# Optimization experiments

Hardware: AMD Instinct MI355X
Metric: run time of the kernel (lower is better)

Reference implementation:

```python
import jax, jax.numpy as jnp
import numpy as np

M = 5            # Anderson memory
LAM = 1e-4       # Tikhonov regularization on Gram matrix
MAX_ITER = 50
TOL = 0.01
BETA = 1.0
BSZ, DIM = 64, 4096


def f_layer(z, x, W, b):
    # canonical DEQ cell: contraction so the fixed point exists
    return jnp.tanh(z @ W + x + b)


def anderson(f, x0, m=M, lam=LAM, max_iter=MAX_ITER, tol=TOL, beta=BETA):
    """Anderson acceleration; faithful port of DEQFixedPoint.anderson.
    Variable history length n=min(k,m) is handled by masking so the whole
    loop is jit-compatible (lax.while_loop with early stop on tol)."""
    bsz = x0.shape[0]
    d = int(np.prod(x0.shape[1:]))
    ff = lambda v: f(v.reshape(x0.shape)).reshape(bsz, d)
    x0f = x0.reshape(bsz, d)

    X = jnp.zeros((bsz, m, d), x0.dtype)
    F = jnp.zeros((bsz, m, d), x0.dtype)
    F0 = ff(x0f)
    F1 = ff(F0)
    X = X.at[:, 0].set(x0f).at[:, 1].set(F0)
    F = F.at[:, 0].set(F0).at[:, 1].set(F1)

    y = jnp.zeros((bsz, m + 1, 1), x0.dtype).at[:, 0, 0].set(1.0)
    eye_m = jnp.eye(m, dtype=x0.dtype)

    def cond(state):
        _, _, k, res = state
        return (k < max_iter) & (res >= tol)

    def body(state):
        X, F, k, res = state
        n = jnp.minimum(k, m)
        mask = (jnp.arange(m) < n).astype(x0.dtype)          # active history slots
        G = (F - X) * mask[None, :, None]                     # (bsz, m, d)
        GG = jnp.einsum('bmd,bnd->bmn', G, G)                 # small 5x5 Gram
        # masked (n+1)x(n+1) subproblem embedded in (m+1)x(m+1): inactive
        # rows become identity rows with zero rhs -> alpha_i = 0 for i >= n,
        # exactly matching torch's solve on the leading (n+1) block.
        Hin = (GG + lam * eye_m) * (mask[:, None] * mask[None, :]) + jnp.diag(1.0 - mask)
        H = jnp.zeros((bsz, m + 1, m + 1), x0.dtype)
        H = H.at[:, 0, 1:].set(mask).at[:, 1:, 0].set(mask).at[:, 1:, 1:].set(Hin)
        alpha = jnp.linalg.solve(H, y)[:, 1:, 0]              # (bsz, m)
        Xk = beta * jnp.einsum('bm,bmd->bd', alpha, F) + (1.0 - beta) * jnp.einsum('bm,bmd->bd', alpha, X)
        Fk = ff(Xk)
        idx = k % m
        Xn = X.at[:, idx].set(Xk)
        Fn = F.at[:, idx].set(Fk)
        r = jnp.linalg.norm(Fk - Xk) / (1e-5 + jnp.linalg.norm(Fk))
        return Xn, Fn, k + 1, r

    init = (X, F, jnp.array(2, jnp.int32), jnp.array(jnp.inf, x0.dtype))
    X, F, k, res = jax.lax.while_loop(cond, body, init)
    idx = (k - 1) % m  # k was incremented after the last executed iteration
    return X[:, idx].reshape(x0.shape)


def setup_inputs():
    key = jax.random.key(0)
    kx, kw, kb = jax.random.split(key, 3)
    x = jax.random.normal(kx, (BSZ, DIM), jnp.float32)
    # spectral norm of W ~ 2 * 0.4 = 0.8 -> contraction through tanh
    W = jax.random.normal(kw, (DIM, DIM), jnp.float32) * (0.4 / np.sqrt(DIM))
    b = jax.random.normal(kb, (DIM,), jnp.float32) * 0.1
    return {"x": x, "W": W, "b": b}


def reference(x, W, b):
    # forward: solve z* = f(z*, x) with no grad, then one grad-carrying f step
    zstar = anderson(lambda z: f_layer(z, x, W, b), jnp.zeros_like(x))
    return f_layer(zstar, x, W, b)
```

## Files before the change

kernel.cpp:

```cpp
#include <hip/hip_runtime.h>

#define NBLK 256
#define GBLK 128
#define NTHR 1024
#define BSZ 64
#define DIM 4096
#define MEM 5
#define MAXIT 50
#define TOL_ 0.01f
#define LAM_ 1e-4f

#define X_OFF 0
#define F_OFF (BSZ * MEM * DIM)
#define Z_OFF (2 * BSZ * MEM * DIM)
#define RP_OFF (Z_OFF + BSZ * DIM)
#define BAR_OFF (RP_OFF + 640)
#define FP32_WS_FLOATS (RP_OFF + 1024)
#define ZF_BYTE ((size_t)(RP_OFF + 1024) * 4)
#define WF_BYTE (ZF_BYTE + (size_t)BSZ * DIM * 2)
#define WS_NEED (WF_BYTE + (size_t)DIM * DIM * 2)

typedef __attribute__((ext_vector_type(8))) _Float16 half8v;
typedef __attribute__((ext_vector_type(4))) float f32x4;

__device__ __forceinline__ unsigned short f2h(float f) {
    _Float16 h = (_Float16)f;
    unsigned short u;
    __builtin_memcpy(&u, &h, 2);
    return u;
}

__device__ __forceinline__ void gridbar(unsigned int* flags, unsigned int* go,
                                        unsigned int e)
{
    __syncthreads();
    const int tid = threadIdx.x;
    if (blockIdx.x == 0) {
        if (tid == 0) {
            __builtin_amdgcn_fence(__ATOMIC_RELEASE, "agent");
            __hip_atomic_store(&flags[0], e, __ATOMIC_RELAXED,
                               __HIP_MEMORY_SCOPE_AGENT);
        }
        if (tid < NBLK) {
            while (__hip_atomic_load(&flags[tid], __ATOMIC_RELAXED,
                                     __HIP_MEMORY_SCOPE_AGENT) < e)
                __builtin_amdgcn_s_sleep(1);
        }
        __syncthreads();
        if (tid == 0) {
            __builtin_amdgcn_fence(__ATOMIC_ACQUIRE, "agent");
            __hip_atomic_store(go, e, __ATOMIC_RELAXED,
                               __HIP_MEMORY_SCOPE_AGENT);
        }
    } else {
        if (tid == 0) {
            __builtin_amdgcn_fence(__ATOMIC_RELEASE, "agent");
            __hip_atomic_store(&flags[blockIdx.x], e, __ATOMIC_RELAXED,
                               __HIP_MEMORY_SCOPE_AGENT);
            while (__hip_atomic_load(go, __ATOMIC_RELAXED,
                                     __HIP_MEMORY_SCOPE_AGENT) < e)
                __builtin_amdgcn_s_sleep(1);
            __builtin_amdgcn_fence(__ATOMIC_ACQUIRE, "agent");
        }
    }
    __syncthreads();
}

__device__ void convert_w(const float* __restrict__ W, unsigned short* __restrict__ Wf,
                          float* smem)
{
    const int tid = threadIdx.x;
    const int blk = blockIdx.x;
    const int jc = blk << 4;
    for (int sc = 0; sc < 8; ++sc) {
        __syncthreads();
        #pragma unroll
        for (int h = 0; h < 2; ++h) {
            int rrow = (tid >> 2) + (h << 8);
            int seg = tid & 3;
            float4 v = *(const float4*)&W[(size_t)((sc << 9) + rrow) * DIM + jc + (seg << 2)];
            float* dst = smem + rrow * 17 + (seg << 2);
            dst[0] = v.x; dst[1] = v.y; dst[2] = v.z; dst[3] = v.w;
        }
        __syncthreads();
        unsigned int* of = (unsigned int*)(Wf + ((size_t)blk * 128 + sc * 16) * 512);
        #pragma unroll
        for (int it = 0; it < 4; ++it) {
            int o = tid + (it << 10);
            int ksl = o >> 8, ln = (o >> 2) & 63, ep = o & 3;
            int kl = (ksl << 5) + ((ln >> 4) << 3) + (ep << 1);
            float w0 = smem[kl * 17 + (ln & 15)];
            float w1 = smem[(kl + 1) * 17 + (ln & 15)];
            of[o] = (unsigned int)f2h(w0) | ((unsigned int)f2h(w1) << 16);
        }
    }
    __syncthreads();
}

__device__ __forceinline__ void gemm_tanh_mfma(
    int idx, const float* __restrict__ x, const float* __restrict__ bias,
    const unsigned short* __restrict__ Zf, const unsigned short* __restrict__ Wf,
    float* __restrict__ Z, float* __restrict__ Fs, float* __restrict__ rp, float* smem)
{
    const int tid = threadIdx.x;
    const int cb = blockIdx.x;
    const int lane = tid & 63;
    const int w = tid >> 6;
    const int r0 = lane & 15;
    const int kg = lane >> 4;
    f32x4 acc[4][2] = {};

    const unsigned short* b0 = Wf + (size_t)(cb * 2) * 65536;
    const unsigned short* b1 = Wf + (size_t)(cb * 2 + 1) * 65536;
    const int ksbase = w << 3;

    #pragma unroll 2
    for (int s = 0; s < 8; ++s) {
        const int ks = ksbase + s;
        const size_t bo = ((size_t)ks << 9) + (lane << 3);
        half8v B0 = *(const half8v*)(b0 + bo);
        half8v B1 = *(const half8v*)(b1 + bo);
        const int kbase = (ks << 5) + (kg << 3);
        #pragma unroll
        for (int m = 0; m < 4; ++m) {
            const size_t ao = (size_t)((m << 4) + r0) * DIM + kbase;
            half8v Ah = *(const half8v*)(Zf + ao);
            acc[m][0] = __builtin_amdgcn_mfma_f32_16x16x32_f16(Ah, B0, acc[m][0], 0, 0, 0);
            acc[m][1] = __builtin_amdgcn_mfma_f32_16x16x32_f16(Ah, B1, acc[m][1], 0, 0, 0);
        }
    }
    const int row = tid >> 4, cc = tid & 15;
    const int m_o = row >> 4, rl = row & 15;
    const int lsrc = cc + ((rl >> 2) << 4), reg = rl & 3;
    float sum0 = 0.f, sum1 = 0.f;
    #pragma unroll
    for (int rnd = 0; rnd < 4; ++rnd) {
        __syncthreads();
        if ((w >> 2) == rnd) {
            float* sec = smem + (w & 3) * 2052;
            #pragma unroll
            for (int m = 0; m < 4; ++m) {
                *(f32x4*)(sec + ((m * 2 + 0) << 8) + (lane << 2)) = acc[m][0];
                *(f32x4*)(sec + ((m * 2 + 1) << 8) + (lane << 2)) = acc[m][1];
            }
        }
        __syncthreads();
        #pragma unroll
        for (int p = 0; p < 4; ++p) {
            sum0 += smem[p * 2052 + ((m_o * 2 + 0) << 8) + (lsrc << 2) + reg];
            sum1 += smem[p * 2052 + ((m_o * 2 + 1) << 8) + (lsrc << 2) + reg];
        }
    }
    const int j0 = (cb << 5) + cc;
    const int j1 = j0 + 16;
    float fz0 = tanhf(sum0 + x[(row << 12) + j0] + bias[j0]);
    float fz1 = tanhf(sum1 + x[(row << 12) + j1] + bias[j1]);
    Fs[(row * MEM + idx) * DIM + j0] = fz0;
    Fs[(row * MEM + idx) * DIM + j1] = fz1;
    float d0 = fz0 - Z[(row << 12) + j0];
    float d1 = fz1 - Z[(row << 12) + j1];
    float lnum = d0 * d0 + d1 * d1;
    float lden = fz0 * fz0 + fz1 * fz1;
    #pragma unroll
    for (int off = 1; off < 64; off <<= 1) {
        lnum += __shfl_xor(lnum, off, 64);
        lden += __shfl_xor(lden, off, 64);
    }
    if (lane == 0) { smem[8448 + w] = lnum; smem[8480 + w] = lden; }
    __syncthreads();
    if (tid == 0) {
        float a = 0.f, b2 = 0.f;
        #pragma unroll
        for (int i = 0; i < 16; ++i) { a += smem[8448 + i]; b2 += smem[8480 + i]; }
        rp[cb] = a;
        rp[NBLK + cb] = b2;
    }
}

__device__ __forceinline__ void gemm_tanh_fp32(
    int idx, const float* __restrict__ x, const float* __restrict__ W,
    const float* __restrict__ bias, float* __restrict__ wsf, float* smem)
{
    const int tid = threadIdx.x;
    const int blk = blockIdx.x;
    const int lane = tid & 63;
    const int w = tid >> 6;
    const int r = w >> 2;
    const int q = w & 3;
    const int jcq = (blk << 4) + (q << 2);
    float* Z = wsf + Z_OFF;
    float* Fs = wsf + F_OFF;
    float* rp = wsf + RP_OFF;

    float acc0 = 0.f, acc1 = 0.f, acc2 = 0.f, acc3 = 0.f;
    const int lx = lane & 15;
    const float* inrow = smem + (r << 12) + (lane << 6);
    const int srow = tid >> 4;
    const int sg = tid & 15;

    for (int step = 0; step < 16; ++step) {
        #pragma unroll
        for (int i = 0; i < 4; ++i) {
            float4 v = *(const float4*)&Z[srow * DIM + (i << 10) + (step << 6) + (sg << 2)];
            *(float4*)&smem[(i << 12) + (srow << 6) + ((sg ^ (srow & 15)) << 2)] = v;
        }
        __syncthreads();
        const float* wbase = W + (size_t)((r << 10) + (step << 6)) * DIM + jcq;
        #pragma unroll 2
        for (int s = 0; s < 16; ++s) {
            float4 in4 = *(const float4*)&inrow[(s ^ lx) << 2];
            const float* wr = wbase + (size_t)(s << 2) * DIM;
            #pragma unroll
            for (int t = 0; t < 4; ++t) {
                float iv = (t == 0) ? in4.x : (t == 1) ? in4.y : (t == 2) ? in4.z : in4.w;
                float4 wq = *(const float4*)(wr + (size_t)t * DIM);
                acc0 = fmaf(iv, wq.x, acc0);
                acc1 = fmaf(iv, wq.y, acc1);
                acc2 = fmaf(iv, wq.z, acc2);
                acc3 = fmaf(iv, wq.w, acc3);
            }
        }
        __syncthreads();
    }
    {
        float* rrow = smem + r * 1088 + lane * 17 + (q << 2);
        rrow[0] = acc0; rrow[1] = acc1; rrow[2] = acc2; rrow[3] = acc3;
    }
    __syncthreads();
    const int row = tid >> 4, cc = tid & 15;
    const int boff = row * 17 + cc;
    float sum = smem[boff] + smem[1088 + boff] + smem[2176 + boff] + smem[3264 + boff];
    const int j = (blk << 4) + cc;
    float fz = tanhf(sum + x[(row << 12) + j] + bias[j]);
    Fs[(row * MEM + idx) * DIM + j] = fz;
    float d = fz - Z[(row << 12) + j];
    float lnum = d * d, lden = fz * fz;
    #pragma unroll
    for (int off = 1; off < 64; off <<= 1) {
        lnum += __shfl_xor(lnum, off, 64);
        lden += __shfl_xor(lden, off, 64);
    }
    if (lane == 0) { smem[8448 + w] = lnum; smem[8480 + w] = lden; }
    __syncthreads();
    if (tid == 0) {
        float a = 0.f, b2 = 0.f;
        for (int i = 0; i < 16; ++i) { a += smem[8448 + i]; b2 += smem[8480 + i]; }
        rp[blk] = a;
        rp[NBLK + blk] = b2;
    }
}

__device__ __forceinline__ float phase_res(const float* __restrict__ rp, float* smem)
{
    const int tid = threadIdx.x;
    const int lane = tid & 63, w = tid >> 6;
    float a = (tid < NBLK) ? rp[tid] : 0.f;
    float b = (tid < NBLK) ? rp[NBLK + tid] : 0.f;
    #pragma unroll
    for (int off = 1; off < 64; off <<= 1) {
        a += __shfl_xor(a, off, 64);
        b += __shfl_xor(b, off, 64);
    }
    if (lane == 0) { smem[w] = a; smem[16 + w] = b; }
    __syncthreads();
    if (tid == 0) {
        float sa = 0.f, sb = 0.f;
        for (int i = 0; i < 16; ++i) { sa += smem[i]; sb += smem[16 + i]; }
        smem[32] = sqrtf(sa) / (1e-5f + sqrtf(sb));
    }
    __syncthreads();
    float res = smem[32];
    __syncthreads();
    return res;
}

template <bool F16>
__device__ void gram_solve_combine(int b, int n, int idx, float* __restrict__ wsf,
                                   unsigned short* __restrict__ Zf, float* smem)
{
    const int tid = threadIdx.x;
    const int lane = tid & 63, w = tid >> 6;
    float* Xs = wsf + X_OFF;
    float* Fs = wsf + F_OFF;
    float* Z = wsf + Z_OFF;
    const int j4 = tid << 2;

    float g[MEM][4];
    #pragma unroll
    for (int i = 0; i < MEM; ++i) {
        float4 fv = *(const float4*)&Fs[(b * MEM + i) * DIM + j4];
        float4 xv = *(const float4*)&Xs[(b * MEM + i) * DIM + j4];
        bool act = (i < n);
        g[i][0] = act ? (fv.x - xv.x) : 0.f;
        g[i][1] = act ? (fv.y - xv.y) : 0.f;
        g[i][2] = act ? (fv.z - xv.z) : 0.f;
        g[i][3] = act ? (fv.w - xv.w) : 0.f;
    }
    float gg[15];
    {
        int p = 0;
        #pragma unroll
        for (int i = 0; i < MEM; ++i)
            #pragma unroll
            for (int qq = i; qq < MEM; ++qq) {
                float s = 0.f;
                #pragma unroll
                for (int c = 0; c < 4; ++c) s = fmaf(g[i][c], g[qq][c], s);
                gg[p++] = s;
            }
    }
    #pragma unroll
    for (int off = 1; off < 64; off <<= 1)
        #pragma unroll
        for (int p = 0; p < 15; ++p) gg[p] += __shfl_xor(gg[p], off, 64);
    if (lane == 0) {
        #pragma unroll
        for (int p = 0; p < 15; ++p) smem[p * 16 + w] = gg[p];
    }
    __syncthreads();
    if (tid == 0) {
        float G[MEM][MEM];
        int p = 0;
        for (int i = 0; i < MEM; ++i)
            for (int qq = i; qq < MEM; ++qq) {
                float v = 0.f;
                for (int ww = 0; ww < 16; ++ww) v += smem[p * 16 + ww];
                G[i][qq] = v; G[qq][i] = v; ++p;
            }
        float H[6][6], yv[6];
        for (int i = 0; i < 6; ++i) yv[i] = (i == 0) ? 1.f : 0.f;
        H[0][0] = 0.f;
        for (int i = 0; i < MEM; ++i) {
            float mi = (i < n) ? 1.f : 0.f;
            H[0][1 + i] = mi;
            H[1 + i][0] = mi;
        }
        for (int i = 0; i < MEM; ++i)
            for (int qq = 0; qq < MEM; ++qq) {
                float v;
                if (i < n && qq < n) v = G[i][qq] + ((i == qq) ? LAM_ : 0.f);
                else v = (i == qq) ? 1.f : 0.f;
                H[1 + i][1 + qq] = v;
            }
        for (int col = 0; col < 6; ++col) {
            int piv = col;
            float mv = fabsf(H[col][col]);
            for (int rr = col + 1; rr < 6; ++rr) {
                float av = fabsf(H[rr][col]);
                if (av > mv) { mv = av; piv = rr; }
            }
            if (piv != col) {
                for (int c2 = 0; c2 < 6; ++c2) { float tv = H[col][c2]; H[col][c2] = H[piv][c2]; H[piv][c2] = tv; }
                float tv = yv[col]; yv[col] = yv[piv]; yv[piv] = tv;
            }
            float pv = H[col][col];
            for (int rr = col + 1; rr < 6; ++rr) {
                float f = H[rr][col] / pv;
                H[rr][col] = 0.f;
                for (int c2 = col + 1; c2 < 6; ++c2) H[rr][c2] -= f * H[col][c2];
                yv[rr] -= f * yv[col];
            }
        }
        float sol[6];
        for (int col = 5; col >= 0; --col) {
            float s = yv[col];
            for (int c2 = col + 1; c2 < 6; ++c2) s -= H[col][c2] * sol[c2];
            sol[col] = s / H[col][col];
        }
        for (int i = 0; i < MEM; ++i) smem[240 + i] = sol[1 + i];
    }
    __syncthreads();
    float al[MEM];
    #pragma unroll
    for (int i = 0; i < MEM; ++i) al[i] = smem[240 + i];
    float4 zf = {0.f, 0.f, 0.f, 0.f};
    #pragma unroll
    for (int i = 0; i < MEM; ++i) {
        float4 fv = *(const float4*)&Fs[(b * MEM + i) * DIM + j4];
        zf.x = fmaf(al[i], fv.x, zf.x);
        zf.y = fmaf(al[i], fv.y, zf.y);
        zf.z = fmaf(al[i], fv.z, zf.z);
        zf.w = fmaf(al[i], fv.w, zf.w);
    }
    *(float4*)&Z[(b << 12) + j4] = zf;
    *(float4*)&Xs[(b * MEM + idx) * DIM + j4] = zf;
    if constexpr (F16) {
        unsigned int* z16 = (unsigned int*)(Zf + ((size_t)b << 12) + j4);
        z16[0] = (unsigned int)f2h(zf.x) | ((unsigned int)f2h(zf.y) << 16);
        z16[1] = (unsigned int)f2h(zf.z) | ((unsigned int)f2h(zf.w) << 16);
    }
}

template <bool F16>
__global__ __launch_bounds__(NTHR, 4)
void deq_anderson(const float* __restrict__ x, const float* __restrict__ W,
                  const float* __restrict__ bias, float* __restrict__ out,
                  char* __restrict__ ws)
{
    __shared__ __align__(16) float smem[16384];
    float* wsf = (float*)ws;
    unsigned int* flags = (unsigned int*)(wsf + BAR_OFF);
    unsigned int* go = flags + 272;
    unsigned short* Zf = (unsigned short*)(ws + ZF_BYTE);
    unsigned short* Wf = (unsigned short*)(ws + WF_BYTE);
    const int tid = threadIdx.x;
    const int blk = blockIdx.x;
    const int e = blk * NTHR + tid;
    const int b = e >> 12, j = e & (DIM - 1);
    float* Xs = wsf + X_OFF;
    float* Fs = wsf + F_OFF;
    float* Z = wsf + Z_OFF;
    float* rp = wsf + RP_OFF;
    unsigned int ep = 1;

    {
        float f0 = tanhf(x[e] + bias[j]);
        #pragma unroll
        for (int i = 0; i < MEM; ++i) {
            Xs[(b * MEM + i) * DIM + j] = (i == 1) ? f0 : 0.f;
            Fs[(b * MEM + i) * DIM + j] = (i == 0) ? f0 : 0.f;
        }
        Z[e] = f0;
        if constexpr (F16) Zf[e] = f2h(f0);
    }
    if constexpr (F16) convert_w(W, Wf, smem);
    gridbar(flags, go, ep++);
    if constexpr (F16) {
        if (blk < GBLK)
            gemm_tanh_mfma(1, x, bias, Zf, Wf, Z, Fs, rp, smem);
        else if (tid == 0) { rp[blk] = 0.f; rp[NBLK + blk] = 0.f; }
    } else {
        gemm_tanh_fp32(1, x, W, bias, wsf, smem);
    }
    gridbar(flags, go, ep++);

    int kend = MAXIT;
    for (int k = 2; k < MAXIT; ++k) {
        float res = phase_res(rp, smem);
        if (k > 2 && res < TOL_) { kend = k; break; }
        const int n = (k < MEM) ? k : MEM;
        const int idx = k % MEM;
        if (blk < BSZ) gram_solve_combine<F16>(blk, n, idx, wsf, Zf, smem);
        gridbar(flags, go, ep++);
        if constexpr (F16) {
            if (blk < GBLK)
                gemm_tanh_mfma(idx, x, bias, Zf, Wf, Z, Fs, rp, smem);
        } else {
            gemm_tanh_fp32(idx, x, W, bias, wsf, smem);
        }
        gridbar(flags, go, ep++);
    }

    const int fidx = (kend - 1) % MEM;
    out[e] = Fs[(b * MEM + fidx) * DIM + j];
}

extern "C" void kernel_launch(void* const* d_in, const int* in_sizes, int n_in,
                              void* d_out, int out_size, void* d_ws, size_t ws_size,
                              hipStream_t stream)
{
    (void)in_sizes; (void)n_in; (void)out_size;
    if (ws_size < (size_t)FP32_WS_FLOATS * sizeof(float)) return;
    const float* x = (const float*)d_in[0];
    const float* W = (const float*)d_in[1];
    const float* b = (const float*)d_in[2];
    float* out = (float*)d_out;
    char* ws = (char*)d_ws;
    hipMemsetAsync(ws + (size_t)BAR_OFF * 4, 0, 1152, stream);
    void* args[] = {(void*)&x, (void*)&W, (void*)&b, (void*)&out, (void*)&ws};
    const void* fn = (ws_size >= WS_NEED)
                         ? reinterpret_cast<const void*>(&deq_anderson<true>)
                         : reinterpret_cast<const void*>(&deq_anderson<false>);
    hipLaunchCooperativeKernel(fn, dim3(NBLK), dim3(NTHR), args, 0, stream);
}
```

Before: 240.4 us.

## Replace two-level grid barrier with all-to-all flag polling; keep F rows in registers

The grid barrier no longer routes through block 0 and a separate go flag. Every block now publishes its epoch flag and polls all 256 flags directly, which removes one serialized round trip per barrier. In exchange, all blocks now generate polling traffic on the shared flag array. Separately, the Anderson combine reuses the F history values already loaded for the Gram computation instead of reloading them from global memory, at the cost of extra registers.

```diff
diff --git a/kernel.cpp b/kernel.cpp
--- a/kernel.cpp
+++ b/kernel.cpp
@@ -30,39 +30,23 @@
     return u;
 }
 
-__device__ __forceinline__ void gridbar(unsigned int* flags, unsigned int* go,
-                                        unsigned int e)
-{
-    __syncthreads();
-    const int tid = threadIdx.x;
-    if (blockIdx.x == 0) {
-        if (tid == 0) {
-            __builtin_amdgcn_fence(__ATOMIC_RELEASE, "agent");
-            __hip_atomic_store(&flags[0], e, __ATOMIC_RELAXED,
-                               __HIP_MEMORY_SCOPE_AGENT);
-        }
-        if (tid < NBLK) {
-            while (__hip_atomic_load(&flags[tid], __ATOMIC_RELAXED,
-                                     __HIP_MEMORY_SCOPE_AGENT) < e)
-                __builtin_amdgcn_s_sleep(1);
-        }
-        __syncthreads();
-        if (tid == 0) {
-            __builtin_amdgcn_fence(__ATOMIC_ACQUIRE, "agent");
-            __hip_atomic_store(go, e, __ATOMIC_RELAXED,
-                               __HIP_MEMORY_SCOPE_AGENT);
-        }
-    } else {
-        if (tid == 0) {
-            __builtin_amdgcn_fence(__ATOMIC_RELEASE, "agent");
-            __hip_atomic_store(&flags[blockIdx.x], e, __ATOMIC_RELAXED,
-                               __HIP_MEMORY_SCOPE_AGENT);
-            while (__hip_atomic_load(go, __ATOMIC_RELAXED,
-                                     __HIP_MEMORY_SCOPE_AGENT) < e)
-                __builtin_amdgcn_s_sleep(1);
-            __builtin_amdgcn_fence(__ATOMIC_ACQUIRE, "agent");
-        }
-    }
+__device__ __forceinline__ void gridbar(unsigned int* flags, unsigned int e)
+{
+    __syncthreads();
+    const int tid = threadIdx.x;
+    if (tid == 0) {
+        __builtin_amdgcn_fence(__ATOMIC_RELEASE, "agent");
+        __hip_atomic_store(&flags[blockIdx.x], e, __ATOMIC_RELAXED,
+                           __HIP_MEMORY_SCOPE_AGENT);
+    }
+    if (tid < NBLK) {
+        while (__hip_atomic_load(&flags[tid], __ATOMIC_RELAXED,
+                                 __HIP_MEMORY_SCOPE_AGENT) < e)
+            __builtin_amdgcn_s_sleep(1);
+    }
+    __syncthreads();
+    if (tid == 0)
+        __builtin_amdgcn_fence(__ATOMIC_ACQUIRE, "agent");
     __syncthreads();
 }
 
@@ -285,16 +269,18 @@
     float* Z = wsf + Z_OFF;
     const int j4 = tid << 2;
 
+    float fv[MEM][4];
     float g[MEM][4];
     #pragma unroll
     for (int i = 0; i < MEM; ++i) {
-        float4 fv = *(const float4*)&Fs[(b * MEM + i) * DIM + j4];
+        float4 f4 = *(const float4*)&Fs[(b * MEM + i) * DIM + j4];
         float4 xv = *(const float4*)&Xs[(b * MEM + i) * DIM + j4];
+        fv[i][0] = f4.x; fv[i][1] = f4.y; fv[i][2] = f4.z; fv[i][3] = f4.w;
         bool act = (i < n);
-        g[i][0] = act ? (fv.x - xv.x) : 0.f;
-        g[i][1] = act ? (fv.y - xv.y) : 0.f;
-        g[i][2] = act ? (fv.z - xv.z) : 0.f;
-        g[i][3] = act ? (fv.w - xv.w) : 0.f;
+        g[i][0] = act ? (f4.x - xv.x) : 0.f;
+        g[i][1] = act ? (f4.y - xv.y) : 0.f;
+        g[i][2] = act ? (f4.z - xv.z) : 0.f;
+        g[i][3] = act ? (f4.w - xv.w) : 0.f;
     }
     float gg[15];
     {
@@ -376,11 +362,10 @@
     float4 zf = {0.f, 0.f, 0.f, 0.f};
     #pragma unroll
     for (int i = 0; i < MEM; ++i) {
-        float4 fv = *(const float4*)&Fs[(b * MEM + i) * DIM + j4];
-        zf.x = fmaf(al[i], fv.x, zf.x);
-        zf.y = fmaf(al[i], fv.y, zf.y);
-        zf.z = fmaf(al[i], fv.z, zf.z);
-        zf.w = fmaf(al[i], fv.w, zf.w);
+        zf.x = fmaf(al[i], fv[i][0], zf.x);
+        zf.y = fmaf(al[i], fv[i][1], zf.y);
+        zf.z = fmaf(al[i], fv[i][2], zf.z);
+        zf.w = fmaf(al[i], fv[i][3], zf.w);
     }
     *(float4*)&Z[(b << 12) + j4] = zf;
     *(float4*)&Xs[(b * MEM + idx) * DIM + j4] = zf;
@@ -400,7 +385,6 @@
     __shared__ __align__(16) float smem[16384];
     float* wsf = (float*)ws;
     unsigned int* flags = (unsigned int*)(wsf + BAR_OFF);
-    unsigned int* go = flags + 272;
     unsigned short* Zf = (unsigned short*)(ws + ZF_BYTE);
     unsigned short* Wf = (unsigned short*)(ws + WF_BYTE);
     const int tid = threadIdx.x;
@@ -424,7 +408,7 @@
         if constexpr (F16) Zf[e] = f2h(f0);
     }
     if constexpr (F16) convert_w(W, Wf, smem);
-    gridbar(flags, go, ep++);
+    gridbar(flags, ep++);
     if constexpr (F16) {
         if (blk < GBLK)
             gemm_tanh_mfma(1, x, bias, Zf, Wf, Z, Fs, rp, smem);
@@ -432,7 +416,7 @@
     } else {
         gemm_tanh_fp32(1, x, W, bias, wsf, smem);
     }
-    gridbar(flags, go, ep++);
+    gridbar(flags, ep++);
 
     int kend = MAXIT;
     for (int k = 2; k < MAXIT; ++k) {
@@ -441,14 +425,14 @@
         const int n = (k < MEM) ? k : MEM;
         const int idx = k % MEM;
         if (blk < BSZ) gram_solve_combine<F16>(blk, n, idx, wsf, Zf, smem);
-        gridbar(flags, go, ep++);
+        gridbar(flags, ep++);
         if constexpr (F16) {
             if (blk < GBLK)
                 gemm_tanh_mfma(idx, x, bias, Zf, Wf, Z, Fs, rp, smem);
         } else {
             gemm_tanh_fp32(idx, x, W, bias, wsf, smem);
         }
-        gridbar(flags, go, ep++);
+        gridbar(flags, ep++);
     }
 
     const int fidx = (kend - 1) % MEM;
@@ -466,7 +450,7 @@
     const float* b = (const float*)d_in[2];
     float* out = (float*)d_out;
     char* ws = (char*)d_ws;
-    hipMemsetAsync(ws + (size_t)BAR_OFF * 4, 0, 1152, stream);
+    hipMemsetAsync(ws + (size_t)BAR_OFF * 4, 0, 1024, stream);
     void* args[] = {(void*)&x, (void*)&W, (void*)&b, (void*)&out, (void*)&ws};
     const void* fn = (ws_size >= WS_NEED)
                          ? reinterpret_cast<const void*>(&deq_anderson<true>)
```

Result: slower. 277.6 us (+15.5%).
